# Kernel tuning notes

Hardware: AMD Instinct MI355X
Metric: run time of the kernel (lower is better)

The kernel has to match this reference:

```python
import jax, jax.numpy as jnp
import numpy as np

B, S, D, H = 64, 512, 1024, 1024


def setup_inputs() -> dict:
    key = jax.random.key(0)
    k1, k2, k3 = jax.random.split(key, 3)
    x = jax.random.normal(k1, (B, S, D), dtype=jnp.float32)
    # torch nn.Linear weight: [4H, D+H], bias: [4H]; scale ~ U-like small init
    W = jax.random.normal(k2, (4 * H, D + H), dtype=jnp.float32) * (1.0 / np.sqrt(D + H))
    b = jax.random.normal(k3, (4 * H,), dtype=jnp.float32) * 0.01
    return {"x": x, "W": W, "b": b}


def reference(x, W, b):
    """BaselineLSTM forward (use_ln=False, dropout=Identity).

    Returns (outputs [B,S,H], (h [B,H], c [B,H])).
    """
    Bv, Sv, Dv = x.shape
    Hv = W.shape[0] // 4
    h0 = jnp.zeros((Bv, Hv), dtype=x.dtype)
    c0 = jnp.zeros((Bv, Hv), dtype=x.dtype)

    def step(carry, x_t):
        h, c = carry
        # gates = Linear(cat([x_t, h])) -> [B, 4H], chunk order i,f,o,g
        gates = jnp.concatenate([x_t, h], axis=1) @ W.T + b
        i, f, o, g = jnp.split(gates, 4, axis=1)
        c_new = jax.nn.sigmoid(f) * c + jax.nn.sigmoid(i) * jnp.tanh(g)
        h_new = jax.nn.sigmoid(o) * jnp.tanh(c_new)
        return (h_new, c_new), h_new

    (h, c), outs = jax.lax.scan(step, (h0, c0), jnp.swapaxes(x, 0, 1))
    outputs = jnp.swapaxes(outs, 0, 1)  # [B, S, H]
    return outputs, (h, c)
```

## Files before the change

### kernel.cpp

```cpp
#include <hip/hip_runtime.h>

typedef unsigned short ushort_t;
typedef unsigned long long u64_t;
typedef float  f32x4  __attribute__((ext_vector_type(4)));
typedef __bf16 bf16x8 __attribute__((ext_vector_type(8)));

#define NB   64
#define NS   512
#define ND   1024
#define NH   1024
#define NG   4096

__device__ __forceinline__ ushort_t f2bf(float f) {
  unsigned u = __float_as_uint(f);
  u += 0x7FFFu + ((u >> 16) & 1u);
  return (ushort_t)(u >> 16);
}
__device__ __forceinline__ float bf2f(ushort_t u) {
  return __uint_as_float(((unsigned)u) << 16);
}
__device__ __forceinline__ float sigmoid_f(float x) {
  return 1.0f / (1.0f + __expf(-x));
}
__device__ __forceinline__ float tanh_f(float x) {
  return 1.0f - 2.0f / (__expf(2.0f * x) + 1.0f);
}

__global__ __launch_bounds__(256) void cvt_x_kernel(const float4* __restrict__ x,
                                                    ushort_t* __restrict__ xb) {
  int i = blockIdx.x * 256 + threadIdx.x;
  float4 v = x[i];
  ushort4 o;
  o.x = f2bf(v.x); o.y = f2bf(v.y); o.z = f2bf(v.z); o.w = f2bf(v.w);
  *(ushort4*)(xb + (size_t)i * 4) = o;
}

__global__ __launch_bounds__(256) void cvt_w_kernel(const float4* __restrict__ W,
                                                    ushort_t* __restrict__ Wx,
                                                    ushort_t* __restrict__ Wh) {
  int i = blockIdx.x * 256 + threadIdx.x;
  float4 v = W[i];
  int e = i * 4;
  int n = e >> 11;
  int c = e & 2047;
  ushort4 o;
  o.x = f2bf(v.x); o.y = f2bf(v.y); o.z = f2bf(v.z); o.w = f2bf(v.w);
  ushort_t* dst = (c < ND) ? (Wx + (size_t)n * ND + c)
                           : (Wh + (size_t)n * NH + (c - ND));
  *(ushort4*)dst = o;
}

__global__ __launch_bounds__(256) void pregemm_kernel(
    const ushort_t* __restrict__ xb, const ushort_t* __restrict__ Wx,
    const float* __restrict__ bias, ushort_t* __restrict__ PG) {
  int bid  = blockIdx.x;
  int mblk = bid >> 5;
  int nblk = bid & 31;
  int tid  = threadIdx.x;
  int lane = tid & 63, w = tid >> 6;
  int l15  = lane & 15, q = lane >> 4;
  int row0 = mblk * 128 + (w >> 1) * 64;
  int col0 = nblk * 128 + (w & 1) * 64;
  const ushort_t* aBase = xb + (size_t)(row0 + l15) * ND + q * 8;
  const ushort_t* bBase = Wx + (size_t)(col0 + l15) * ND + q * 8;

  f32x4 acc[4][4] = {};
#pragma unroll 2
  for (int k0 = 0; k0 < ND; k0 += 32) {
    bf16x8 a[4], b[4];
#pragma unroll
    for (int mi = 0; mi < 4; ++mi)
      a[mi] = *reinterpret_cast<const bf16x8*>(aBase + (size_t)mi * 16 * ND + k0);
#pragma unroll
    for (int ni = 0; ni < 4; ++ni)
      b[ni] = *reinterpret_cast<const bf16x8*>(bBase + (size_t)ni * 16 * ND + k0);
#pragma unroll
    for (int mi = 0; mi < 4; ++mi)
#pragma unroll
      for (int ni = 0; ni < 4; ++ni)
        acc[mi][ni] = __builtin_amdgcn_mfma_f32_16x16x32_bf16(a[mi], b[ni], acc[mi][ni], 0, 0, 0);
  }
#pragma unroll
  for (int ni = 0; ni < 4; ++ni) {
    int n = col0 + ni * 16 + l15;
    float bv = bias[n];
#pragma unroll
    for (int mi = 0; mi < 4; ++mi) {
#pragma unroll
      for (int r = 0; r < 4; ++r) {
        int m  = row0 + mi * 16 + q * 4 + r;
        int bb = m >> 9;
        int t  = m & 511;
        PG[((size_t)t * NB + bb) * NG + n] = f2bf(acc[mi][ni][r] + bv);
      }
    }
  }
}

__global__ __launch_bounds__(1024) void lstm_rec_kernel(
    const ushort_t* __restrict__ PG, const ushort_t* __restrict__ Wh,
    ushort_t* hbuf, unsigned* cnt, float* __restrict__ out) {
  __shared__ ushort_t lds_h[64 * 1024];
  __shared__ float lds_g[4][64][17];

  int bid = blockIdx.x;
  int j0  = bid * 16;
  int tid = threadIdx.x;
  int lane = tid & 63, w = tid >> 6;
  int g = w & 3, ms = w >> 2;
  int l15 = lane & 15, q = lane >> 4;
  int jj = tid & 15, m = tid >> 4;

  const ushort_t* bB = Wh + (size_t)(g * NH + j0 + l15) * NH + q * 8;

  int rowA = ms * 16 + l15;
  int swA  = (rowA & 7) << 4;
  const char* aRow = (const char*)lds_h + rowA * 2048;

  float c_reg = 0.f;

  ushort_t pg0, pg1, pg2, pg3;
  {
    const ushort_t* pp = PG + (size_t)m * NG + j0 + jj;
    pg0 = __builtin_nontemporal_load(pp);
    pg1 = __builtin_nontemporal_load(pp + NH);
    pg2 = __builtin_nontemporal_load(pp + 2 * NH);
    pg3 = __builtin_nontemporal_load(pp + 3 * NH);
  }

  for (int t = 0; t < NS; ++t) {
    if (t > 0) {
      if (tid == 0) {
        unsigned tgt = 64u * (unsigned)t;
        int guard = 0;
        while (__hip_atomic_load(cnt, __ATOMIC_RELAXED, __HIP_MEMORY_SCOPE_AGENT) < tgt) {
          if (++guard > (1 << 14)) break;
        }
      }
      __builtin_amdgcn_sched_barrier(0);
      __syncthreads();
    }

    {
      const u64_t* hb64 = (const u64_t*)(hbuf + (size_t)(t & 1) * (NB * NH));
      u64_t hv8[16];
#pragma unroll
      for (int it = 0; it < 16; ++it)
        hv8[it] = __hip_atomic_load(hb64 + it * 1024 + tid,
                                    __ATOMIC_RELAXED, __HIP_MEMORY_SCOPE_AGENT);
#pragma unroll
      for (int it = 0; it < 16; ++it) {
        int idx  = it * 1024 + tid;
        int row  = idx >> 8;
        int colB = (idx & 255) * 8;
        *(u64_t*)((char*)lds_h + row * 2048 + (colB ^ ((row & 7) << 4))) = hv8[it];
      }
    }
    __syncthreads();

    f32x4 acc = {};
#pragma unroll 8
    for (int k0 = 0; k0 < NH; k0 += 32) {
      bf16x8 av = *(const bf16x8*)(aRow + ((16 * q + 2 * k0) ^ swA));
      bf16x8 bv = *reinterpret_cast<const bf16x8*>(bB + k0);
      acc = __builtin_amdgcn_mfma_f32_16x16x32_bf16(av, bv, acc, 0, 0, 0);
    }
#pragma unroll
    for (int r = 0; r < 4; ++r)
      lds_g[g][ms * 16 + q * 4 + r][l15] = acc[r];
    __syncthreads();

    float gi = lds_g[0][m][jj] + bf2f(pg0);
    float gf = lds_g[1][m][jj] + bf2f(pg1);
    float go = lds_g[2][m][jj] + bf2f(pg2);
    float gg = lds_g[3][m][jj] + bf2f(pg3);
    float cn = sigmoid_f(gf) * c_reg + sigmoid_f(gi) * tanh_f(gg);
    float hv = sigmoid_f(go) * tanh_f(cn);
    c_reg = cn;

    unsigned my16 = (unsigned)f2bf(hv);
    unsigned nb16 = (unsigned)__shfl_down((int)my16, 1);
    if (t == NS - 1) {
      out[((size_t)m * NS + t) * NH + j0 + jj] = hv;
      out[(size_t)NB * NS * NH + (size_t)m * NH + j0 + jj] = hv;
      out[(size_t)NB * NS * NH + (size_t)NB * NH + (size_t)m * NH + j0 + jj] = cn;
    } else {
      if ((tid & 1) == 0) {
        unsigned* hn32 = (unsigned*)(hbuf + (size_t)((t & 1) ^ 1) * (NB * NH));
        __hip_atomic_store(hn32 + m * (NH / 2) + ((j0 + jj) >> 1),
                           my16 | (nb16 << 16),
                           __ATOMIC_RELAXED, __HIP_MEMORY_SCOPE_AGENT);
      }
      __syncthreads();
      if (tid == 0)
        __hip_atomic_fetch_add(cnt, 1u, __ATOMIC_RELAXED, __HIP_MEMORY_SCOPE_AGENT);
      __builtin_nontemporal_store(hv, &out[((size_t)m * NS + t) * NH + j0 + jj]);
      const ushort_t* pn = PG + ((size_t)(t + 1) * NB + m) * NG + j0 + jj;
      pg0 = __builtin_nontemporal_load(pn);
      pg1 = __builtin_nontemporal_load(pn + NH);
      pg2 = __builtin_nontemporal_load(pn + 2 * NH);
      pg3 = __builtin_nontemporal_load(pn + 3 * NH);
    }
  }
}

extern "C" void kernel_launch(void* const* d_in, const int* in_sizes, int n_in,
                              void* d_out, int out_size, void* d_ws, size_t ws_size,
                              hipStream_t stream) {
  const float* x    = (const float*)d_in[0];
  const float* W    = (const float*)d_in[1];
  const float* bias = (const float*)d_in[2];
  float* out = (float*)d_out;

  const size_t off_hbuf = 0;
  const size_t off_cnt  = 262144;
  const size_t off_Wx   = 262272;
  const size_t off_Wh   = off_Wx + 8388608;
  const size_t off_xb   = off_Wh + 8388608;
  const size_t off_PG   = off_xb + 67108864;
  const size_t need     = off_PG + 268435456;
  if (ws_size < need) return;

  char* ws = (char*)d_ws;
  ushort_t* hbuf = (ushort_t*)(ws + off_hbuf);
  unsigned* cnt  = (unsigned*)(ws + off_cnt);
  ushort_t* Wx   = (ushort_t*)(ws + off_Wx);
  ushort_t* Wh   = (ushort_t*)(ws + off_Wh);
  ushort_t* xb   = (ushort_t*)(ws + off_xb);
  ushort_t* PG   = (ushort_t*)(ws + off_PG);

  hipMemsetAsync(ws, 0, 262272, stream);

  cvt_x_kernel<<<32768, 256, 0, stream>>>((const float4*)x, xb);
  cvt_w_kernel<<<8192, 256, 0, stream>>>((const float4*)W, Wx, Wh);
  pregemm_kernel<<<8192, 256, 0, stream>>>(xb, Wx, bias, PG);

  void* args[] = { (void*)&PG, (void*)&Wh, (void*)&hbuf, (void*)&cnt, (void*)&out };
  hipLaunchCooperativeKernel((void*)lstm_rec_kernel, dim3(64), dim3(1024),
                             args, 0, stream);
}
```

Baseline: 10.53 ms.

## Split recurrence into independent batch groups with per-block step flags

Result: faster. 9.533 ms (-9.5%).

```diff
diff --git a/kernel.cpp b/kernel.cpp
--- a/kernel.cpp
+++ b/kernel.cpp
@@ -99,29 +99,37 @@
 
 __global__ __launch_bounds__(1024) void lstm_rec_kernel(
     const ushort_t* __restrict__ PG, const ushort_t* __restrict__ Wh,
-    ushort_t* hbuf, unsigned* cnt, float* __restrict__ out) {
-  __shared__ ushort_t lds_h[64 * 1024];
-  __shared__ float lds_g[4][64][17];
-
-  int bid = blockIdx.x;
-  int j0  = bid * 16;
-  int tid = threadIdx.x;
+    ushort_t* hbuf, unsigned* flags, float* __restrict__ out) {
+  __shared__ ushort_t lds_h[16 * 1024];
+  __shared__ float lds_g[4][16][66];
+
+  int bid  = blockIdx.x;
+  int mach = bid >> 4;
+  int slot = bid & 15;
+  int tid  = threadIdx.x;
   int lane = tid & 63, w = tid >> 6;
-  int g = w & 3, ms = w >> 2;
+  int g = w & 3, jb = w >> 2;
   int l15 = lane & 15, q = lane >> 4;
-  int jj = tid & 15, m = tid >> 4;
-
-  const ushort_t* bB = Wh + (size_t)(g * NH + j0 + l15) * NH + q * 8;
-
-  int rowA = ms * 16 + l15;
-  int swA  = (rowA & 7) << 4;
-  const char* aRow = (const char*)lds_h + rowA * 2048;
-
+  int mb = tid >> 6, jc = tid & 63;
+
+  ushort_t* hm0 = hbuf + (size_t)(mach * 2) * (16 * NH);
+  ushort_t* hm1 = hm0 + 16 * NH;
+
+  const ushort_t* bB =
+      Wh + (size_t)(g * NH + slot * 64 + jb * 16 + l15) * NH + q * 8;
+
+  int swA = (l15 & 7) << 4;
+  const char* aRow = (const char*)lds_h + l15 * 2048;
+
+  unsigned* myflag = flags + (size_t)(mach * 16 + slot) * 32;
   float c_reg = 0.f;
+
+  int bglob = mach * 16 + mb;
+  int jglob = slot * 64 + jc;
 
   ushort_t pg0, pg1, pg2, pg3;
   {
-    const ushort_t* pp = PG + (size_t)m * NG + j0 + jj;
+    const ushort_t* pp = PG + (size_t)bglob * NG + jglob;
     pg0 = __builtin_nontemporal_load(pp);
     pg1 = __builtin_nontemporal_load(pp + NH);
     pg2 = __builtin_nontemporal_load(pp + 2 * NH);
@@ -130,10 +138,14 @@
 
   for (int t = 0; t < NS; ++t) {
     if (t > 0) {
-      if (tid == 0) {
-        unsigned tgt = 64u * (unsigned)t;
+      if (w == 0) {
+        unsigned tgt = (unsigned)t;
+        const unsigned* fp = flags + (size_t)(mach * 16 + (lane & 15)) * 32;
         int guard = 0;
-        while (__hip_atomic_load(cnt, __ATOMIC_RELAXED, __HIP_MEMORY_SCOPE_AGENT) < tgt) {
+        for (;;) {
+          unsigned v = __hip_atomic_load(fp, __ATOMIC_RELAXED,
+                                         __HIP_MEMORY_SCOPE_AGENT);
+          if (__all(v >= tgt)) break;
           if (++guard > (1 << 14)) break;
         }
       }
@@ -142,14 +154,15 @@
     }
 
     {
-      const u64_t* hb64 = (const u64_t*)(hbuf + (size_t)(t & 1) * (NB * NH));
-      u64_t hv8[16];
-#pragma unroll
-      for (int it = 0; it < 16; ++it)
+      const u64_t* hb64 =
+          (const u64_t*)((t & 1) ? hm1 : hm0);
+      u64_t hv8[4];
+#pragma unroll
+      for (int it = 0; it < 4; ++it)
         hv8[it] = __hip_atomic_load(hb64 + it * 1024 + tid,
                                     __ATOMIC_RELAXED, __HIP_MEMORY_SCOPE_AGENT);
 #pragma unroll
-      for (int it = 0; it < 16; ++it) {
+      for (int it = 0; it < 4; ++it) {
         int idx  = it * 1024 + tid;
         int row  = idx >> 8;
         int colB = (idx & 255) * 8;
@@ -167,13 +180,13 @@
     }
 #pragma unroll
     for (int r = 0; r < 4; ++r)
-      lds_g[g][ms * 16 + q * 4 + r][l15] = acc[r];
+      lds_g[g][q * 4 + r][jb * 16 + l15] = acc[r];
     __syncthreads();
 
-    float gi = lds_g[0][m][jj] + bf2f(pg0);
-    float gf = lds_g[1][m][jj] + bf2f(pg1);
-    float go = lds_g[2][m][jj] + bf2f(pg2);
-    float gg = lds_g[3][m][jj] + bf2f(pg3);
+    float gi = lds_g[0][mb][jc] + bf2f(pg0);
+    float gf = lds_g[1][mb][jc] + bf2f(pg1);
+    float go = lds_g[2][mb][jc] + bf2f(pg2);
+    float gg = lds_g[3][mb][jc] + bf2f(pg3);
     float cn = sigmoid_f(gf) * c_reg + sigmoid_f(gi) * tanh_f(gg);
     float hv = sigmoid_f(go) * tanh_f(cn);
     c_reg = cn;
@@ -181,21 +194,22 @@
     unsigned my16 = (unsigned)f2bf(hv);
     unsigned nb16 = (unsigned)__shfl_down((int)my16, 1);
     if (t == NS - 1) {
-      out[((size_t)m * NS + t) * NH + j0 + jj] = hv;
-      out[(size_t)NB * NS * NH + (size_t)m * NH + j0 + jj] = hv;
-      out[(size_t)NB * NS * NH + (size_t)NB * NH + (size_t)m * NH + j0 + jj] = cn;
+      out[((size_t)bglob * NS + t) * NH + jglob] = hv;
+      out[(size_t)NB * NS * NH + (size_t)bglob * NH + jglob] = hv;
+      out[(size_t)NB * NS * NH + (size_t)NB * NH + (size_t)bglob * NH + jglob] = cn;
     } else {
       if ((tid & 1) == 0) {
-        unsigned* hn32 = (unsigned*)(hbuf + (size_t)((t & 1) ^ 1) * (NB * NH));
-        __hip_atomic_store(hn32 + m * (NH / 2) + ((j0 + jj) >> 1),
+        unsigned* hn32 = (unsigned*)((t & 1) ? hm0 : hm1);
+        __hip_atomic_store(hn32 + mb * 512 + slot * 32 + (jc >> 1),
                            my16 | (nb16 << 16),
                            __ATOMIC_RELAXED, __HIP_MEMORY_SCOPE_AGENT);
       }
       __syncthreads();
       if (tid == 0)
-        __hip_atomic_fetch_add(cnt, 1u, __ATOMIC_RELAXED, __HIP_MEMORY_SCOPE_AGENT);
-      __builtin_nontemporal_store(hv, &out[((size_t)m * NS + t) * NH + j0 + jj]);
-      const ushort_t* pn = PG + ((size_t)(t + 1) * NB + m) * NG + j0 + jj;
+        __hip_atomic_store(myflag, (unsigned)(t + 1),
+                           __ATOMIC_RELAXED, __HIP_MEMORY_SCOPE_AGENT);
+      __builtin_nontemporal_store(hv, &out[((size_t)bglob * NS + t) * NH + jglob]);
+      const ushort_t* pn = PG + ((size_t)(t + 1) * NB + bglob) * NG + jglob;
       pg0 = __builtin_nontemporal_load(pn);
       pg1 = __builtin_nontemporal_load(pn + NH);
       pg2 = __builtin_nontemporal_load(pn + 2 * NH);
@@ -212,30 +226,30 @@
   const float* bias = (const float*)d_in[2];
   float* out = (float*)d_out;
 
-  const size_t off_hbuf = 0;
-  const size_t off_cnt  = 262144;
-  const size_t off_Wx   = 262272;
-  const size_t off_Wh   = off_Wx + 8388608;
-  const size_t off_xb   = off_Wh + 8388608;
-  const size_t off_PG   = off_xb + 67108864;
-  const size_t need     = off_PG + 268435456;
+  const size_t off_hbuf  = 0;
+  const size_t off_flags = 262144;
+  const size_t off_Wx    = 270336;
+  const size_t off_Wh    = off_Wx + 8388608;
+  const size_t off_xb    = off_Wh + 8388608;
+  const size_t off_PG    = off_xb + 67108864;
+  const size_t need      = off_PG + 268435456;
   if (ws_size < need) return;
 
   char* ws = (char*)d_ws;
-  ushort_t* hbuf = (ushort_t*)(ws + off_hbuf);
-  unsigned* cnt  = (unsigned*)(ws + off_cnt);
-  ushort_t* Wx   = (ushort_t*)(ws + off_Wx);
-  ushort_t* Wh   = (ushort_t*)(ws + off_Wh);
-  ushort_t* xb   = (ushort_t*)(ws + off_xb);
-  ushort_t* PG   = (ushort_t*)(ws + off_PG);
-
-  hipMemsetAsync(ws, 0, 262272, stream);
+  ushort_t* hbuf  = (ushort_t*)(ws + off_hbuf);
+  unsigned* flags = (unsigned*)(ws + off_flags);
+  ushort_t* Wx    = (ushort_t*)(ws + off_Wx);
+  ushort_t* Wh    = (ushort_t*)(ws + off_Wh);
+  ushort_t* xb    = (ushort_t*)(ws + off_xb);
+  ushort_t* PG    = (ushort_t*)(ws + off_PG);
+
+  hipMemsetAsync(ws, 0, 270336, stream);
 
   cvt_x_kernel<<<32768, 256, 0, stream>>>((const float4*)x, xb);
   cvt_w_kernel<<<8192, 256, 0, stream>>>((const float4*)W, Wx, Wh);
   pregemm_kernel<<<8192, 256, 0, stream>>>(xb, Wx, bias, PG);
 
-  void* args[] = { (void*)&PG, (void*)&Wh, (void*)&hbuf, (void*)&cnt, (void*)&out };
+  void* args[] = { (void*)&PG, (void*)&Wh, (void*)&hbuf, (void*)&flags, (void*)&out };
   hipLaunchCooperativeKernel((void*)lstm_rec_kernel, dim3(64), dim3(1024),
                              args, 0, stream);
 }
```
